# Optimization experiments

Hardware: AMD Instinct MI355X
Metric: run time of the kernel (lower is better)

## Reference

```python
import jax, jax.numpy as jnp
import numpy as np

EPS_NORM = 1e-12
BN_EPS = 1e-5
TEMP = 0.07


def _l2norm(x, axis):
    n = jnp.sqrt(jnp.sum(x * x, axis=axis, keepdims=True))
    return x / jnp.maximum(n, EPS_NORM)


def _bn_eval(z, w, b):
    # inference-mode BatchNorm2d with running_mean=0, running_var=1
    s = w / jnp.sqrt(jnp.asarray(1.0 + BN_EPS, z.dtype))
    return z * s[None, :, None, None] + b[None, :, None, None]


def setup_inputs() -> dict:
    key = jax.random.key(0)
    ks = jax.random.split(key, 8)
    B, C, H, W = 16, 256, 64, 64
    KD, P = 128, 256
    x = jax.random.normal(ks[0], (B, C, H, W), jnp.float32)
    m_features = jax.random.normal(ks[1], (P, KD), jnp.float32)
    q_w = jax.random.normal(ks[2], (KD, C), jnp.float32) * 0.05
    k_w = jax.random.normal(ks[3], (KD, KD), jnp.float32) * 0.05
    v_w = jax.random.normal(ks[4], (KD, KD), jnp.float32) * 0.05
    o_w = jax.random.normal(ks[5], (C, KD), jnp.float32) * 0.05
    dw_w = jax.random.normal(ks[6], (C, 1, 3, 3), jnp.float32) * 0.1
    return {
        "x": x, "m_features": m_features,
        "q_w": q_w, "q_b": jnp.zeros((KD,), jnp.float32),
        "k_w": k_w, "k_b": jnp.zeros((KD,), jnp.float32),
        "v_w": v_w, "v_b": jnp.zeros((KD,), jnp.float32),
        "o_w": o_w, "o_b": jnp.zeros((C,), jnp.float32),
        "dw_w": dw_w,
        "bn1_w": jnp.ones((C,), jnp.float32), "bn1_b": jnp.zeros((C,), jnp.float32),
        "bn2_w": jnp.ones((C,), jnp.float32), "bn2_b": jnp.zeros((C,), jnp.float32),
        "gamma": jnp.ones((C,), jnp.float32) * 1e-5,
    }


def reference(x, m_features, q_w, q_b, k_w, k_b, v_w, v_b, o_w, o_b,
              dw_w, bn1_w, bn1_b, bn2_w, bn2_b, gamma):
    B, C, H, W = x.shape
    KD = q_w.shape[0]
    residual = x
    # q_proj 1x1 conv -> [B,KD,H,W], L2-normalize over channel dim
    q = jnp.einsum('bchw,kc->bkhw', x, q_w) + q_b[None, :, None, None]
    q = _l2norm(q, axis=1)
    q = q.reshape(B, KD, H * W).transpose(0, 2, 1)  # [B, HW, KD]
    # k/v projections of memory bank [P, KD]
    k = _l2norm(m_features @ k_w.T + k_b, axis=-1)
    v = m_features @ v_w.T + v_b
    # fp32 attention with clamped logits
    q32, k32, v32 = q.astype(jnp.float32), k.astype(jnp.float32), v.astype(jnp.float32)
    logits = jnp.clip(jnp.einsum('bnd,pd->bnp', q32, k32) / TEMP, -30.0, 30.0)
    attn = jax.nn.softmax(logits, axis=-1)
    out = jnp.einsum('bnp,pd->bnd', attn, v32).astype(x.dtype)
    out = out.transpose(0, 2, 1).reshape(B, KD, H, W)
    # out_proj 1x1 conv -> [B,C,H,W]
    out = jnp.einsum('bkhw,ck->bchw', out, o_w) + o_b[None, :, None, None]
    # local branch: depthwise 3x3 conv + BN + exact GELU
    local = jax.lax.conv_general_dilated(
        out, dw_w, window_strides=(1, 1), padding='SAME',
        feature_group_count=C,
        dimension_numbers=('NCHW', 'OIHW', 'NCHW'))
    local = jax.nn.gelu(_bn_eval(local, bn1_w, bn1_b), approximate=False)
    out = out + local
    return _bn_eval(residual + out * gamma[None, :, None, None], bn2_w, bn2_b)
```

## Files before the change

### kernel.cpp

```cpp
#include <hip/hip_runtime.h>
#include <hip/hip_bf16.h>
#include <math.h>

#define B_ 16
#define C_ 256
#define H_ 64
#define W_ 64
#define KD_ 128
#define P_ 256
#define HW_ (H_ * W_)

typedef __bf16 bf16;
typedef float f32x4_t __attribute__((ext_vector_type(4)));
typedef float f32x16_t __attribute__((ext_vector_type(16)));
typedef unsigned char u8;

__device__ __forceinline__ unsigned cvt_pk_fp8_lo(float a, float b, unsigned old) {
#if __has_builtin(__builtin_amdgcn_cvt_pk_fp8_f32)
    return __builtin_amdgcn_cvt_pk_fp8_f32(a, b, old, false);
#else
    unsigned r = old;
    asm("v_cvt_pk_fp8_f32 %0, %1, %2" : "+v"(r) : "v"(a), "v"(b));
    return r;
#endif
}
__device__ __forceinline__ unsigned cvt_pk_fp8_hi(float a, float b, unsigned old) {
#if __has_builtin(__builtin_amdgcn_cvt_pk_fp8_f32)
    return __builtin_amdgcn_cvt_pk_fp8_f32(a, b, old, true);
#else
    unsigned r = old;
    asm("v_cvt_pk_fp8_f32 %0, %1, %2 op_sel:[0,0,1]" : "+v"(r) : "v"(a), "v"(b));
    return r;
#endif
}
__device__ __forceinline__ uint2 pack8_fp8(const float* f) {
    uint2 r;
    r.x = cvt_pk_fp8_hi(f[2], f[3], cvt_pk_fp8_lo(f[0], f[1], 0u));
    r.y = cvt_pk_fp8_hi(f[6], f[7], cvt_pk_fp8_lo(f[4], f[5], 0u));
    return r;
}
template<int SEL>
__device__ __forceinline__ float fp8_to_f32(unsigned w) {
#if __has_builtin(__builtin_amdgcn_cvt_f32_fp8)
    return __builtin_amdgcn_cvt_f32_fp8(w, SEL);
#else
    float r;
    asm("v_cvt_f32_fp8 %0, %1" : "=v"(r) : "v"(w >> (SEL * 8)));
    return r;
#endif
}

__global__ __launch_bounds__(512, 8) void k_xpose(
    const float* __restrict__ x, u8* __restrict__ x8)
{
    __shared__ __align__(16) u8 tile[16 * 2048];
    const int cblk = blockIdx.x >> 1;
    const int ph   = blockIdx.x & 1;
    const int b    = blockIdx.y;
    const int t = threadIdx.x;

    {
        const int cl = t >> 5, sub = t & 31;
        const float* src = x + ((size_t)b * C_ + cblk * 16 + cl) * HW_ + ph * 2048;
#pragma unroll
        for (int i = 0; i < 16; ++i) {
            const f32x4_t v = *(const f32x4_t*)(src + (i * 32 + sub) * 4);
            const unsigned w = cvt_pk_fp8_hi(v[2], v[3],
                               cvt_pk_fp8_lo(v[0], v[1], 0u));
            *(unsigned*)&tile[cl * 2048 + (i * 32 + sub) * 4] = w;
        }
    }
    __syncthreads();
    {
        const int pr = t & 63;
        const int r0 = t >> 6;
#pragma unroll
        for (int it = 0; it < 4; ++it) {
            const int r = it * 8 + r0;
            const int lp = r * 64 + pr;
            union { u8 bytes[16]; uint4 u; } g;
#pragma unroll
            for (int c = 0; c < 16; ++c) g.bytes[c] = tile[c * 2048 + lp];
            const int h = ph * 32 + r;
            *(uint4*)(x8 + (((size_t)(b * 64 + h) * 16 + cblk) << 10) + pr * 16) = g.u;
        }
    }
}

__global__ __launch_bounds__(128) void k_prep1(
    const float* __restrict__ m_feat,
    const float* __restrict__ k_w, const float* __restrict__ k_b,
    const float* __restrict__ v_w, const float* __restrict__ v_b,
    float* __restrict__ kn_f, float* __restrict__ v_f)
{
    const int p = blockIdx.x;
    const int j = threadIdx.x;
    __shared__ float msh[KD_];
    __shared__ float red[2];
    msh[j] = m_feat[p * KD_ + j];
    __syncthreads();

    float ka = k_b[j];
    float va = v_b[j];
#pragma unroll 4
    for (int d = 0; d < KD_; ++d) {
        const float m = msh[d];
        ka = fmaf(m, k_w[j * KD_ + d], ka);
        va = fmaf(m, v_w[j * KD_ + d], va);
    }
    float s = ka * ka;
#pragma unroll
    for (int o = 1; o < 64; o <<= 1) s += __shfl_xor(s, o);
    if ((j & 63) == 0) red[j >> 6] = s;
    __syncthreads();
    s = red[0] + red[1];
    const float inv = 1.0f / (0.07f * fmaxf(sqrtf(s), 1e-12f));
    kn_f[p * KD_ + j] = ka * inv;
    v_f[p * KD_ + j] = va;
}

__global__ __launch_bounds__(256) void k_prep23(
    const float* __restrict__ o_w, const float* __restrict__ v_f,
    const float* __restrict__ q_w, const float* __restrict__ kn_f,
    u8* __restrict__ m28, u8* __restrict__ qw8, u8* __restrict__ kn8)
{
    if (blockIdx.x < 256) {
        const int c = blockIdx.x;
        const int p = threadIdx.x;
        __shared__ float osh[KD_];
        if (p < KD_) osh[p] = o_w[c * KD_ + p];
        __syncthreads();
        float acc = 0.f;
#pragma unroll 4
        for (int k = 0; k < KD_; ++k) acc = fmaf(osh[k], v_f[p * KD_ + k], acc);
        const int mt = c >> 5, r = c & 31;
        const int ks = p >> 4, sub = (p >> 3) & 1, jj = p & 7;
        const unsigned pk = cvt_pk_fp8_lo(acc * 16.0f, 0.f, 0u);
        m28[(((mt * 16 + ks) * 64) + sub * 32 + r) * 8 + jj] = (u8)(pk & 0xffu);
    } else {
        const int t = (blockIdx.x - 256) * 256 + threadIdx.x;
        float f[8];
        if (t < 4096) {
            const int lane = t & 63, g = t >> 6, mt = g >> 4, ks = g & 15;
            const int row = mt * 32 + (lane & 31), k0 = ks * 16 + (lane >> 5) * 8;
            const float* src = q_w + row * C_ + k0;
#pragma unroll
            for (int j = 0; j < 8; ++j) f[j] = src[j] * 16.0f;
            ((uint2*)qw8)[t] = pack8_fp8(f);
        } else {
            const int u = t - 4096;
            const int lane = u & 63, g = u >> 6, mt = g >> 3, ks = g & 7;
            const int row = mt * 32 + (lane & 31), k0 = ks * 16 + (lane >> 5) * 8;
            const float* src = kn_f + row * KD_ + k0;
#pragma unroll
            for (int j = 0; j < 8; ++j) f[j] = src[j];
            ((uint2*)kn8)[u] = pack8_fp8(f);
        }
    }
}

__global__ __launch_bounds__(512, 4) void k_attn(
    const u8* __restrict__ x8,
    const float* __restrict__ q_b, const float* __restrict__ o_b,
    const u8* __restrict__ qw8, const u8* __restrict__ kn8,
    const u8* __restrict__ m28, u8* __restrict__ outf8)
{
    __shared__ __align__(16) char lds[43008];
    char* const ebuf = lds;
    char* const qbuf = lds + 16384;
    float* const ss_lds   = (float*)(lds + 32768);
    float* const pmax_lds = (float*)(lds + 34816);
    float* const sum_lds  = (float*)(lds + 38912);

    const int rp = blockIdx.x;
    const int b = blockIdx.y;
    const int tid = threadIdx.x;
    const int lane = tid & 63;
    const int wid = tid >> 6;
    const int l31 = lane & 31;
    const int kh  = lane >> 5;

    const int mtA = wid & 3, nh = wid >> 2;
    {
        const u8* xrow = x8 + ((size_t)(b * 64 + rp * 2 + nh) << 14);
        f32x16_t qacc0, qacc1;
#pragma unroll
        for (int i = 0; i < 16; ++i) { qacc0[i] = 0.f; qacc1[i] = 0.f; }
#pragma unroll
        for (int ks = 0; ks < 16; ++ks) {
            const long a = *(const long*)(qw8 + ((mtA * 16 + ks) * 64 + lane) * 8);
            const long bx0 = *(const long*)(xrow + ks * 1024 + l31 * 16 + kh * 8);
            const long bx1 = *(const long*)(xrow + ks * 1024 + (32 + l31) * 16 + kh * 8);
            qacc0 = __builtin_amdgcn_mfma_f32_32x32x16_fp8_fp8(a, bx0, qacc0, 0, 0, 0);
            qacc1 = __builtin_amdgcn_mfma_f32_32x32x16_fp8_fp8(a, bx1, qacc1, 0, 0, 0);
        }
#pragma unroll
        for (int nt = 0; nt < 2; ++nt) {
            const int pix = nh * 64 + nt * 32 + l31;
            float ssp = 0.f;
#pragma unroll
            for (int g = 0; g < 4; ++g) {
                const f32x4_t qbv = *(const f32x4_t*)(q_b + mtA * 32 + g * 8 + kh * 4);
#pragma unroll
                for (int i = 0; i < 4; ++i) {
                    float qv = (nt == 0) ? qacc0[g * 4 + i] : qacc1[g * 4 + i];
                    qv += 16.0f * qbv[i];
                    if (nt == 0) qacc0[g * 4 + i] = qv; else qacc1[g * 4 + i] = qv;
                    ssp = fmaf(qv, qv, ssp);
                }
            }
            ssp += __shfl_xor(ssp, 32);
            if (lane < 32) ss_lds[pix * 4 + mtA] = ssp;
#pragma unroll
            for (int g = 0; g < 4; ++g) {
                const float e0 = (nt == 0) ? qacc0[g * 4 + 0] : qacc1[g * 4 + 0];
                const float e1 = (nt == 0) ? qacc0[g * 4 + 1] : qacc1[g * 4 + 1];
                const float e2 = (nt == 0) ? qacc0[g * 4 + 2] : qacc1[g * 4 + 2];
                const float e3 = (nt == 0) ? qacc0[g * 4 + 3] : qacc1[g * 4 + 3];
                const unsigned qw_ = cvt_pk_fp8_hi(e2, e3, cvt_pk_fp8_lo(e0, e1, 0u));
                *(unsigned*)(qbuf + pix * 128 +
                             ((mtA * 32 + g * 8 + kh * 4) ^ ((l31 & 15) << 3))) = qw_;
            }
        }
    }
    __syncthreads();

    f32x16_t lacc0, lacc1, lacc2, lacc3;
#pragma unroll
    for (int i = 0; i < 16; ++i) { lacc0[i] = 0.f; lacc1[i] = 0.f; lacc2[i] = 0.f; lacc3[i] = 0.f; }
#pragma unroll
    for (int ks = 0; ks < 8; ++ks) {
        const long a = *(const long*)(kn8 + ((wid * 8 + ks) * 64 + lane) * 8);
        const int ko = (ks * 16 + kh * 8) ^ ((l31 & 15) << 3);
        const long bq0 = *(const long*)(qbuf + (0 * 32 + l31) * 128 + ko);
        const long bq1 = *(const long*)(qbuf + (1 * 32 + l31) * 128 + ko);
        const long bq2 = *(const long*)(qbuf + (2 * 32 + l31) * 128 + ko);
        const long bq3 = *(const long*)(qbuf + (3 * 32 + l31) * 128 + ko);
        lacc0 = __builtin_amdgcn_mfma_f32_32x32x16_fp8_fp8(a, bq0, lacc0, 0, 0, 0);
        lacc1 = __builtin_amdgcn_mfma_f32_32x32x16_fp8_fp8(a, bq1, lacc1, 0, 0, 0);
        lacc2 = __builtin_amdgcn_mfma_f32_32x32x16_fp8_fp8(a, bq2, lacc2, 0, 0, 0);
        lacc3 = __builtin_amdgcn_mfma_f32_32x32x16_fp8_fp8(a, bq3, lacc3, 0, 0, 0);
    }
#pragma unroll
    for (int nt = 0; nt < 4; ++nt) {
        const int pix = nt * 32 + l31;
        float mx = -1e30f;
#pragma unroll
        for (int i = 0; i < 16; ++i) {
            const float lv = (nt == 0) ? lacc0[i] : (nt == 1) ? lacc1[i]
                           : (nt == 2) ? lacc2[i] : lacc3[i];
            mx = fmaxf(mx, lv);
        }
        mx = fmaxf(mx, __shfl_xor(mx, 32));
        if (lane < 32) pmax_lds[pix * 8 + wid] = mx;
    }
    __syncthreads();

#pragma unroll
    for (int nt = 0; nt < 4; ++nt) {
        const int pix = nt * 32 + l31;
        const f32x4_t s4 = *(const f32x4_t*)(ss_lds + pix * 4);
        const float qinv = 1.0f / fmaxf(sqrtf(s4[0] + s4[1] + s4[2] + s4[3]), 1e-12f);
        const f32x4_t ma = *(const f32x4_t*)(pmax_lds + pix * 8);
        const f32x4_t mb = *(const f32x4_t*)(pmax_lds + pix * 8 + 4);
        const float cof = 5.545177444479562f -
                          fmaxf(fmaxf(fmaxf(ma[0], ma[1]), fmaxf(ma[2], ma[3])),
                                fmaxf(fmaxf(mb[0], mb[1]), fmaxf(mb[2], mb[3]))) * qinv;
        float sm = 0.f;
#pragma unroll
        for (int g = 0; g < 4; ++g) {
            float e[4];
#pragma unroll
            for (int i = 0; i < 4; ++i) {
                const float lv = (nt == 0) ? lacc0[g * 4 + i] : (nt == 1) ? lacc1[g * 4 + i]
                               : (nt == 2) ? lacc2[g * 4 + i] : lacc3[g * 4 + i];
                e[i] = __expf(fmaf(lv, qinv, cof));
                sm += e[i];
            }
            const unsigned ew = cvt_pk_fp8_hi(e[2], e[3],
                                cvt_pk_fp8_lo(e[0], e[1], 0u));
            const int p0 = wid * 32 + g * 8 + kh * 4;
            *(unsigned*)(ebuf + pix * 256 + (p0 ^ (l31 << 3))) = ew;
        }
        sm += __shfl_xor(sm, 32);
        if (lane < 32) sum_lds[pix * 8 + wid] = sm;
    }
    __syncthreads();

    f32x16_t oacc0, oacc1, oacc2, oacc3;
#pragma unroll
    for (int i = 0; i < 16; ++i) { oacc0[i] = 0.f; oacc1[i] = 0.f; oacc2[i] = 0.f; oacc3[i] = 0.f; }
#pragma unroll
    for (int ks = 0; ks < 16; ++ks) {
        const long a = *(const long*)(m28 + ((wid * 16 + ks) * 64 + lane) * 8);
        const int ko = (ks * 16 + kh * 8);
        const long be0 = *(const long*)(ebuf + (0 * 32 + l31) * 256 + (ko ^ (l31 << 3)));
        const long be1 = *(const long*)(ebuf + (1 * 32 + l31) * 256 + (ko ^ (l31 << 3)));
        const long be2 = *(const long*)(ebuf + (2 * 32 + l31) * 256 + (ko ^ (l31 << 3)));
        const long be3 = *(const long*)(ebuf + (3 * 32 + l31) * 256 + (ko ^ (l31 << 3)));
        oacc0 = __builtin_amdgcn_mfma_f32_32x32x16_fp8_fp8(a, be0, oacc0, 0, 0, 0);
        oacc1 = __builtin_amdgcn_mfma_f32_32x32x16_fp8_fp8(a, be1, oacc1, 0, 0, 0);
        oacc2 = __builtin_amdgcn_mfma_f32_32x32x16_fp8_fp8(a, be2, oacc2, 0, 0, 0);
        oacc3 = __builtin_amdgcn_mfma_f32_32x32x16_fp8_fp8(a, be3, oacc3, 0, 0, 0);
    }
    {
        u8* const obase = outf8 + (size_t)b * C_ * HW_ + rp * 128;
        f32x4_t obv16[4];
#pragma unroll
        for (int g = 0; g < 4; ++g) {
            const f32x4_t t = *(const f32x4_t*)(o_b + wid * 32 + g * 8 + kh * 4);
            obv16[g] = t * 16.0f;
        }
#pragma unroll
        for (int nt = 0; nt < 4; ++nt) {
            const int p = nt * 32 + l31;
            const f32x4_t sa = *(const f32x4_t*)(sum_lds + p * 8);
            const f32x4_t sb = *(const f32x4_t*)(sum_lds + p * 8 + 4);
            const float rs16 = 1.0f / ((sa[0] + sa[1] + sa[2] + sa[3]) +
                                       (sb[0] + sb[1] + sb[2] + sb[3]));
            u8* const op = obase + p;
#pragma unroll
            for (int g = 0; g < 4; ++g) {
                float o[4];
#pragma unroll
                for (int i = 0; i < 4; ++i) {
                    const float av = (nt == 0) ? oacc0[g * 4 + i] : (nt == 1) ? oacc1[g * 4 + i]
                                   : (nt == 2) ? oacc2[g * 4 + i] : oacc3[g * 4 + i];
                    o[i] = fmaf(av, rs16, obv16[g][i]);
                }
                const unsigned u01 = cvt_pk_fp8_lo(o[0], o[1], 0u);
                const unsigned u23 = cvt_pk_fp8_lo(o[2], o[3], 0u);
                const int c = wid * 32 + g * 8 + kh * 4;
                op[(size_t)(c + 0) * HW_] = (u8)(u01 & 0xff);
                op[(size_t)(c + 1) * HW_] = (u8)((u01 >> 8) & 0xff);
                op[(size_t)(c + 2) * HW_] = (u8)(u23 & 0xff);
                op[(size_t)(c + 3) * HW_] = (u8)((u23 >> 8) & 0xff);
            }
        }
    }
}

__global__ __launch_bounds__(256, 4) void k_post(
    const float* __restrict__ x, const u8* __restrict__ outf8,
    const float* __restrict__ dw_w,
    const float* __restrict__ bn1_w, const float* __restrict__ bn1_b,
    const float* __restrict__ bn2_w, const float* __restrict__ bn2_b,
    const float* __restrict__ gamma, float* __restrict__ y)
{
    __shared__ __align__(16) u8 os8[64 + HW_ + 64];
    u8* const os = os8 + 64;
    const int bc = blockIdx.x;
    const int c = bc & (C_ - 1);
    const int tid = threadIdx.x;

    if (tid < 4)       *(uint4*)&os8[tid * 16] = make_uint4(0, 0, 0, 0);
    else if (tid < 8)  *(uint4*)&os8[64 + HW_ + (tid - 4) * 16] = make_uint4(0, 0, 0, 0);
    *(uint4*)&os[tid * 16] = *(const uint4*)(outf8 + (size_t)bc * HW_ + tid * 16);

    const float cbn = 0.99999500003750f;
    const float s1 = bn1_w[c] * cbn, b1 = bn1_b[c];
    const float s2 = bn2_w[c] * cbn, b2 = bn2_b[c];
    const float g = gamma[c];
    const float gc = g * 0.0625f;
    float kw[9];
#pragma unroll
    for (int j = 0; j < 9; ++j) kw[j] = dw_w[c * 9 + j] * 0.0625f;

    __syncthreads();

    const int q = tid & 15;
    const int c4 = q * 4;
    const int r0 = tid >> 4;
    const float* xc = x + (size_t)bc * HW_;
    float* yc = y + (size_t)bc * HW_;

#pragma unroll
    for (int k = 0; k < 4; ++k) {
        const int r = r0 + k * 16;
        const f32x4_t x4 = *(const f32x4_t*)(xc + r * 64 + c4);
        float vt[6], vm[6], vb[6];
        {
            const int rbt = r * 64, rbm = rbt + 64, rbb = rbt + 128;
            const unsigned uCt = *(const unsigned*)&os8[rbt + c4];
            const unsigned uCm = *(const unsigned*)&os8[rbm + c4];
            const unsigned uCb = *(const unsigned*)&os8[rbb + c4];
            vt[1] = fp8_to_f32<0>(uCt); vt[2] = fp8_to_f32<1>(uCt);
            vt[3] = fp8_to_f32<2>(uCt); vt[4] = fp8_to_f32<3>(uCt);
            vm[1] = fp8_to_f32<0>(uCm); vm[2] = fp8_to_f32<1>(uCm);
            vm[3] = fp8_to_f32<2>(uCm); vm[4] = fp8_to_f32<3>(uCm);
            vb[1] = fp8_to_f32<0>(uCb); vb[2] = fp8_to_f32<1>(uCb);
            vb[3] = fp8_to_f32<2>(uCb); vb[4] = fp8_to_f32<3>(uCb);
            if (q > 0) {
                vt[0] = fp8_to_f32<3>(*(const unsigned*)&os8[rbt + c4 - 4]);
                vm[0] = fp8_to_f32<3>(*(const unsigned*)&os8[rbm + c4 - 4]);
                vb[0] = fp8_to_f32<3>(*(const unsigned*)&os8[rbb + c4 - 4]);
            } else { vt[0] = vm[0] = vb[0] = 0.f; }
            if (q < 15) {
                vt[5] = fp8_to_f32<0>(*(const unsigned*)&os8[rbt + c4 + 4]);
                vm[5] = fp8_to_f32<0>(*(const unsigned*)&os8[rbm + c4 + 4]);
                vb[5] = fp8_to_f32<0>(*(const unsigned*)&os8[rbb + c4 + 4]);
            } else { vt[5] = vm[5] = vb[5] = 0.f; }
        }
        f32x4_t y4;
#pragma unroll
        for (int j = 0; j < 4; ++j) {
            float conv = kw[0] * vt[j];
            conv = fmaf(kw[1], vt[j + 1], conv);
            conv = fmaf(kw[2], vt[j + 2], conv);
            conv = fmaf(kw[3], vm[j], conv);
            conv = fmaf(kw[4], vm[j + 1], conv);
            conv = fmaf(kw[5], vm[j + 2], conv);
            conv = fmaf(kw[6], vb[j], conv);
            conv = fmaf(kw[7], vb[j + 1], conv);
            conv = fmaf(kw[8], vb[j + 2], conv);
            const float t = fmaf(conv, s1, b1);
            const float lg = t / (1.0f + __expf(-1.702f * t));
            y4[j] = fmaf(lg, g, fmaf(vm[j + 1], gc, x4[j])) * s2 + b2;
        }
        *(f32x4_t*)(yc + r * 64 + c4) = y4;
    }
}

extern "C" void kernel_launch(void* const* d_in, const int* in_sizes, int n_in,
                              void* d_out, int out_size, void* d_ws, size_t ws_size,
                              hipStream_t stream)
{
    const float* x     = (const float*)d_in[0];
    const float* m_f   = (const float*)d_in[1];
    const float* q_w   = (const float*)d_in[2];
    const float* q_b   = (const float*)d_in[3];
    const float* k_w   = (const float*)d_in[4];
    const float* k_b   = (const float*)d_in[5];
    const float* v_w   = (const float*)d_in[6];
    const float* v_b   = (const float*)d_in[7];
    const float* o_w   = (const float*)d_in[8];
    const float* o_b   = (const float*)d_in[9];
    const float* dw_w  = (const float*)d_in[10];
    const float* bn1_w = (const float*)d_in[11];
    const float* bn1_b = (const float*)d_in[12];
    const float* bn2_w = (const float*)d_in[13];
    const float* bn2_b = (const float*)d_in[14];
    const float* gamma = (const float*)d_in[15];

    char* ws = (char*)d_ws;
    u8*    qw8   = (u8*)(ws);
    u8*    kn8   = (u8*)(ws + (32 << 10));
    u8*    m28   = (u8*)(ws + (64 << 10));
    u8*    x8    = (u8*)(ws + (1 << 20));
    u8*    outf8 = (u8*)(ws + (17 << 20));
    float* kn_f  = (float*)(ws + (34 << 20));
    float* v_f   = (float*)(ws + (34 << 20) + (128 << 10));

    k_xpose<<<dim3(32, B_), dim3(512), 0, stream>>>(x, x8);
    k_prep1<<<dim3(P_), dim3(128), 0, stream>>>(m_f, k_w, k_b, v_w, v_b,
                                                kn_f, v_f);
    k_prep23<<<dim3(288), dim3(256), 0, stream>>>(o_w, v_f, q_w, kn_f,
                                                  m28, qw8, kn8);
    k_attn<<<dim3(H_ / 2, B_), dim3(512), 0, stream>>>(x8, q_b, o_b, qw8, kn8,
                                                       m28, outf8);
    k_post<<<dim3(B_ * C_), dim3(256), 0, stream>>>(
        x, outf8, dw_w, bn1_w, bn1_b, bn2_w, bn2_b, gamma, (float*)d_out);
}
```

Before: 81.25 us.

## Fuse fp8 transpose of x into attention kernel via LDS staging

```diff
diff --git a/kernel.cpp b/kernel.cpp
--- a/kernel.cpp
+++ b/kernel.cpp
@@ -48,43 +48,6 @@
     asm("v_cvt_f32_fp8 %0, %1" : "=v"(r) : "v"(w >> (SEL * 8)));
     return r;
 #endif
-}
-
-__global__ __launch_bounds__(512, 8) void k_xpose(
-    const float* __restrict__ x, u8* __restrict__ x8)
-{
-    __shared__ __align__(16) u8 tile[16 * 2048];
-    const int cblk = blockIdx.x >> 1;
-    const int ph   = blockIdx.x & 1;
-    const int b    = blockIdx.y;
-    const int t = threadIdx.x;
-
-    {
-        const int cl = t >> 5, sub = t & 31;
-        const float* src = x + ((size_t)b * C_ + cblk * 16 + cl) * HW_ + ph * 2048;
-#pragma unroll
-        for (int i = 0; i < 16; ++i) {
-            const f32x4_t v = *(const f32x4_t*)(src + (i * 32 + sub) * 4);
-            const unsigned w = cvt_pk_fp8_hi(v[2], v[3],
-                               cvt_pk_fp8_lo(v[0], v[1], 0u));
-            *(unsigned*)&tile[cl * 2048 + (i * 32 + sub) * 4] = w;
-        }
-    }
-    __syncthreads();
-    {
-        const int pr = t & 63;
-        const int r0 = t >> 6;
-#pragma unroll
-        for (int it = 0; it < 4; ++it) {
-            const int r = it * 8 + r0;
-            const int lp = r * 64 + pr;
-            union { u8 bytes[16]; uint4 u; } g;
-#pragma unroll
-            for (int c = 0; c < 16; ++c) g.bytes[c] = tile[c * 2048 + lp];
-            const int h = ph * 32 + r;
-            *(uint4*)(x8 + (((size_t)(b * 64 + h) * 16 + cblk) << 10) + pr * 16) = g.u;
-        }
-    }
 }
 
 __global__ __launch_bounds__(128) void k_prep1(
@@ -160,17 +123,16 @@
 }
 
 __global__ __launch_bounds__(512, 4) void k_attn(
-    const u8* __restrict__ x8,
+    const float* __restrict__ x,
     const float* __restrict__ q_b, const float* __restrict__ o_b,
     const u8* __restrict__ qw8, const u8* __restrict__ kn8,
     const u8* __restrict__ m28, u8* __restrict__ outf8)
 {
-    __shared__ __align__(16) char lds[43008];
-    char* const ebuf = lds;
-    char* const qbuf = lds + 16384;
-    float* const ss_lds   = (float*)(lds + 32768);
-    float* const pmax_lds = (float*)(lds + 34816);
-    float* const sum_lds  = (float*)(lds + 38912);
+    __shared__ __align__(16) char lds[75776];
+    char* const xs = lds + 32768;
+    float* const ss_lds   = (float*)(lds + 65536);
+    float* const pmax_lds = (float*)(lds + 67584);
+    float* const sum_lds  = (float*)(lds + 71680);
 
     const int rp = blockIdx.x;
     const int b = blockIdx.y;
@@ -180,17 +142,52 @@
     const int l31 = lane & 31;
     const int kh  = lane >> 5;
 
+    long kna[8];
+#pragma unroll
+    for (int ks = 0; ks < 8; ++ks)
+        kna[ks] = *(const long*)(kn8 + ((wid * 8 + ks) * 64 + lane) * 8);
+
+    {
+        const int sub = tid & 31;
+        const int ch0 = tid >> 5;
+        const float* xb = x + (size_t)b * C_ * HW_ + rp * 128 + sub * 4;
+#pragma unroll
+        for (int it = 0; it < 16; ++it) {
+            const int ch = it * 16 + ch0;
+            const f32x4_t v = *(const f32x4_t*)(xb + (size_t)ch * HW_);
+            const unsigned w = cvt_pk_fp8_hi(v[2], v[3],
+                               cvt_pk_fp8_lo(v[0], v[1], 0u));
+            *(unsigned*)(lds + ch * 128 + sub * 4) = w;
+        }
+    }
+    __syncthreads();
+
+    {
+        const int p  = tid & 127;
+        const int cb = tid >> 7;
+#pragma unroll
+        for (int g = 0; g < 8; ++g) {
+            const int c0 = cb * 64 + g * 8;
+            union { u8 by[8]; uint2 u; } pk;
+#pragma unroll
+            for (int j = 0; j < 8; ++j)
+                pk.by[j] = *(const u8*)(lds + (c0 + j) * 128 + p);
+            *(uint2*)(xs + p * 256 + (c0 ^ ((p & 31) << 3))) = pk.u;
+        }
+    }
+    __syncthreads();
+
     const int mtA = wid & 3, nh = wid >> 2;
     {
-        const u8* xrow = x8 + ((size_t)(b * 64 + rp * 2 + nh) << 14);
         f32x16_t qacc0, qacc1;
 #pragma unroll
         for (int i = 0; i < 16; ++i) { qacc0[i] = 0.f; qacc1[i] = 0.f; }
 #pragma unroll
         for (int ks = 0; ks < 16; ++ks) {
             const long a = *(const long*)(qw8 + ((mtA * 16 + ks) * 64 + lane) * 8);
-            const long bx0 = *(const long*)(xrow + ks * 1024 + l31 * 16 + kh * 8);
-            const long bx1 = *(const long*)(xrow + ks * 1024 + (32 + l31) * 16 + kh * 8);
+            const int ko = (ks * 16 + kh * 8) ^ (l31 << 3);
+            const long bx0 = *(const long*)(xs + (nh * 64 + l31) * 256 + ko);
+            const long bx1 = *(const long*)(xs + (nh * 64 + 32 + l31) * 256 + ko);
             qacc0 = __builtin_amdgcn_mfma_f32_32x32x16_fp8_fp8(a, bx0, qacc0, 0, 0, 0);
             qacc1 = __builtin_amdgcn_mfma_f32_32x32x16_fp8_fp8(a, bx1, qacc1, 0, 0, 0);
         }
@@ -218,7 +215,7 @@
                 const float e2 = (nt == 0) ? qacc0[g * 4 + 2] : qacc1[g * 4 + 2];
                 const float e3 = (nt == 0) ? qacc0[g * 4 + 3] : qacc1[g * 4 + 3];
                 const unsigned qw_ = cvt_pk_fp8_hi(e2, e3, cvt_pk_fp8_lo(e0, e1, 0u));
-                *(unsigned*)(qbuf + pix * 128 +
+                *(unsigned*)(lds + pix * 128 +
                              ((mtA * 32 + g * 8 + kh * 4) ^ ((l31 & 15) << 3))) = qw_;
             }
         }
@@ -230,16 +227,15 @@
     for (int i = 0; i < 16; ++i) { lacc0[i] = 0.f; lacc1[i] = 0.f; lacc2[i] = 0.f; lacc3[i] = 0.f; }
 #pragma unroll
     for (int ks = 0; ks < 8; ++ks) {
-        const long a = *(const long*)(kn8 + ((wid * 8 + ks) * 64 + lane) * 8);
         const int ko = (ks * 16 + kh * 8) ^ ((l31 & 15) << 3);
-        const long bq0 = *(const long*)(qbuf + (0 * 32 + l31) * 128 + ko);
-        const long bq1 = *(const long*)(qbuf + (1 * 32 + l31) * 128 + ko);
-        const long bq2 = *(const long*)(qbuf + (2 * 32 + l31) * 128 + ko);
-        const long bq3 = *(const long*)(qbuf + (3 * 32 + l31) * 128 + ko);
-        lacc0 = __builtin_amdgcn_mfma_f32_32x32x16_fp8_fp8(a, bq0, lacc0, 0, 0, 0);
-        lacc1 = __builtin_amdgcn_mfma_f32_32x32x16_fp8_fp8(a, bq1, lacc1, 0, 0, 0);
-        lacc2 = __builtin_amdgcn_mfma_f32_32x32x16_fp8_fp8(a, bq2, lacc2, 0, 0, 0);
-        lacc3 = __builtin_amdgcn_mfma_f32_32x32x16_fp8_fp8(a, bq3, lacc3, 0, 0, 0);
+        const long bq0 = *(const long*)(lds + (0 * 32 + l31) * 128 + ko);
+        const long bq1 = *(const long*)(lds + (1 * 32 + l31) * 128 + ko);
+        const long bq2 = *(const long*)(lds + (2 * 32 + l31) * 128 + ko);
+        const long bq3 = *(const long*)(lds + (3 * 32 + l31) * 128 + ko);
+        lacc0 = __builtin_amdgcn_mfma_f32_32x32x16_fp8_fp8(kna[ks], bq0, lacc0, 0, 0, 0);
+        lacc1 = __builtin_amdgcn_mfma_f32_32x32x16_fp8_fp8(kna[ks], bq1, lacc1, 0, 0, 0);
+        lacc2 = __builtin_amdgcn_mfma_f32_32x32x16_fp8_fp8(kna[ks], bq2, lacc2, 0, 0, 0);
+        lacc3 = __builtin_amdgcn_mfma_f32_32x32x16_fp8_fp8(kna[ks], bq3, lacc3, 0, 0, 0);
     }
 #pragma unroll
     for (int nt = 0; nt < 4; ++nt) {
@@ -280,7 +276,7 @@
             const unsigned ew = cvt_pk_fp8_hi(e[2], e[3],
                                 cvt_pk_fp8_lo(e[0], e[1], 0u));
             const int p0 = wid * 32 + g * 8 + kh * 4;
-            *(unsigned*)(ebuf + pix * 256 + (p0 ^ (l31 << 3))) = ew;
+            *(unsigned*)(lds + pix * 256 + (p0 ^ (l31 << 3))) = ew;
         }
         sm += __shfl_xor(sm, 32);
         if (lane < 32) sum_lds[pix * 8 + wid] = sm;
@@ -294,10 +290,10 @@
     for (int ks = 0; ks < 16; ++ks) {
         const long a = *(const long*)(m28 + ((wid * 16 + ks) * 64 + lane) * 8);
         const int ko = (ks * 16 + kh * 8);
-        const long be0 = *(const long*)(ebuf + (0 * 32 + l31) * 256 + (ko ^ (l31 << 3)));
-        const long be1 = *(const long*)(ebuf + (1 * 32 + l31) * 256 + (ko ^ (l31 << 3)));
-        const long be2 = *(const long*)(ebuf + (2 * 32 + l31) * 256 + (ko ^ (l31 << 3)));
-        const long be3 = *(const long*)(ebuf + (3 * 32 + l31) * 256 + (ko ^ (l31 << 3)));
+        const long be0 = *(const long*)(lds + (0 * 32 + l31) * 256 + (ko ^ (l31 << 3)));
+        const long be1 = *(const long*)(lds + (1 * 32 + l31) * 256 + (ko ^ (l31 << 3)));
+        const long be2 = *(const long*)(lds + (2 * 32 + l31) * 256 + (ko ^ (l31 << 3)));
+        const long be3 = *(const long*)(lds + (3 * 32 + l31) * 256 + (ko ^ (l31 << 3)));
         oacc0 = __builtin_amdgcn_mfma_f32_32x32x16_fp8_fp8(a, be0, oacc0, 0, 0, 0);
         oacc1 = __builtin_amdgcn_mfma_f32_32x32x16_fp8_fp8(a, be1, oacc1, 0, 0, 0);
         oacc2 = __builtin_amdgcn_mfma_f32_32x32x16_fp8_fp8(a, be2, oacc2, 0, 0, 0);
@@ -446,17 +442,15 @@
     u8*    qw8   = (u8*)(ws);
     u8*    kn8   = (u8*)(ws + (32 << 10));
     u8*    m28   = (u8*)(ws + (64 << 10));
-    u8*    x8    = (u8*)(ws + (1 << 20));
-    u8*    outf8 = (u8*)(ws + (17 << 20));
-    float* kn_f  = (float*)(ws + (34 << 20));
-    float* v_f   = (float*)(ws + (34 << 20) + (128 << 10));
-
-    k_xpose<<<dim3(32, B_), dim3(512), 0, stream>>>(x, x8);
+    u8*    outf8 = (u8*)(ws + (1 << 20));
+    float* kn_f  = (float*)(ws + (1 << 20));
+    float* v_f   = (float*)(ws + (1 << 20) + (128 << 10));
+
     k_prep1<<<dim3(P_), dim3(128), 0, stream>>>(m_f, k_w, k_b, v_w, v_b,
                                                 kn_f, v_f);
     k_prep23<<<dim3(288), dim3(256), 0, stream>>>(o_w, v_f, q_w, kn_f,
                                                   m28, qw8, kn8);
-    k_attn<<<dim3(H_ / 2, B_), dim3(512), 0, stream>>>(x8, q_b, o_b, qw8, kn8,
+    k_attn<<<dim3(H_ / 2, B_), dim3(512), 0, stream>>>(x, q_b, o_b, qw8, kn8,
                                                        m28, outf8);
     k_post<<<dim3(B_ * C_), dim3(256), 0, stream>>>(
         x, outf8, dw_w, bn1_w, bn1_b, bn2_w, bn2_b, gamma, (float*)d_out);
```

Result: faster. 73.99 us (-8.9%).
